# Kernel tuning notes

Measured on AMD Instinct MI355X. Metric: run time of the kernel, lower is better.

Reference implementation:

```python
import math
import jax, jax.numpy as jnp
import numpy as np

N, CH3, T = 64, 192, 2048

def setup_inputs() -> dict:
    key = jax.random.key(0)
    qkv = jax.random.normal(key, (N, CH3, T), dtype=jnp.float32)
    return {"qkv": qkv}

def reference(qkv):
    ch = qkv.shape[1] // 3
    q, k, v = jnp.split(qkv, 3, axis=1)  # each [b, c, t]
    scale = 1.0 / math.sqrt(math.sqrt(ch))
    # [b, t, s] score matrix (faithful to the naive implementation)
    weight = jnp.einsum('bct,bcs->bts', q * scale, k * scale)
    weight = jax.nn.softmax(weight.astype(jnp.float32), axis=-1).astype(weight.dtype)
    return jnp.einsum('bts,bcs->bct', weight, v)
```

## Files before the change

### kernel.cpp

```cpp
#include <hip/hip_runtime.h>
#include <math.h>


#define B_     64
#define CH_    64
#define T_     2048
#define TQ     128
#define SB     64
#define NIT    (T_ / SB)
#define TILE_E 4096

typedef __attribute__((ext_vector_type(8))) short short8;
typedef __attribute__((ext_vector_type(4))) float f32x4;
typedef __attribute__((ext_vector_type(16))) float f32x16;
typedef __attribute__((ext_vector_type(4))) unsigned short us4;
typedef __attribute__((ext_vector_type(8))) unsigned short us8;

static __device__ __forceinline__ unsigned short f2bf(float f) {
    union { float f; unsigned u; } v; v.f = f;
    unsigned r = v.u + 0x7FFFu + ((v.u >> 16) & 1u);
    return (unsigned short)(r >> 16);
}

static __device__ __forceinline__ short8 ld_contig(const unsigned short* p) {
    return *(const short8*)p;
}

static __device__ __forceinline__ short8 ld_strided(const unsigned short* p, int stride) {
    short8 r;
#pragma unroll
    for (int j = 0; j < 8; ++j) r[j] = (short)p[j * stride];
    return r;
}

static __device__ __forceinline__ void gl_lds16(const unsigned short* g, unsigned short* l) {
    __builtin_amdgcn_global_load_lds(
        (const __attribute__((address_space(1))) unsigned int*)g,
        (__attribute__((address_space(3))) unsigned int*)l, 16, 0, 0);
}

static __device__ __forceinline__ float vexp2(float x) {
#if __has_builtin(__builtin_amdgcn_exp2f)
    return __builtin_amdgcn_exp2f(x);
#else
    float r;
    asm("v_exp_f32 %0, %1\n\ts_nop 1" : "=v"(r) : "v"(x));
    return r;
#endif
}

static __device__ __forceinline__ unsigned cvtpk(float lo, float hi) {
    unsigned r;
    asm("v_cvt_pk_bf16_f32 %0, %1, %2" : "=v"(r) : "v"(lo), "v"(hi));
    return r;
}

static __device__ __forceinline__ void pl32(unsigned& a, unsigned& b) {
    asm("v_permlane32_swap_b32 %0, %1" : "+v"(a), "+v"(b));
}

static __device__ __forceinline__ void pl_swap(unsigned& a, unsigned& b) {
    asm("v_permlane32_swap_b32 %0, %1" : "+v"(a), "+v"(b));
    asm("v_permlane16_swap_b32 %0, %1" : "+v"(a), "+v"(b));
}

__global__ __launch_bounds__(256) void qkv_prep(const float* __restrict__ qkv,
                                                unsigned short* __restrict__ Ktg,
                                                unsigned short* __restrict__ Vbg)
{
    __shared__ float Tl[64][65];
    const int tid = threadIdx.x;
    const int b   = blockIdx.x >> 5;
    const int st  = blockIdx.x & 31;
    const int s0  = st * 64;
    const float* Kp = qkv + (size_t)b * (3 * CH_ * T_) + (size_t)CH_ * T_;
    const float* Vp = Kp + (size_t)CH_ * T_;
    const size_t tbase = (size_t)(b * 32 + st) * TILE_E;

    {
        const int c = tid & 63, fq = tid >> 6;
#pragma unroll
        for (int k = 0; k < 4; ++k) {
            const int tl = 16 * fq + 4 * k;
            const float4 v = *(const float4*)(Kp + (size_t)c * T_ + s0 + tl);
            Tl[c][tl] = v.x; Tl[c][tl + 1] = v.y; Tl[c][tl + 2] = v.z; Tl[c][tl + 3] = v.w;
        }
    }

    {
        const int c = tid >> 2, tq = (tid & 3) * 16;
        unsigned short* vout = Vbg + (size_t)b * CH_ * T_ + (size_t)c * T_ + s0 + tq;
        const float* vin = Vp + (size_t)c * T_ + s0 + tq;
#pragma unroll
        for (int k = 0; k < 2; ++k) {
            const float4 a  = *(const float4*)(vin + 8 * k);
            const float4 bq = *(const float4*)(vin + 8 * k + 4);
            us8 w8;
            w8[0]=f2bf(a.x);  w8[1]=f2bf(a.y);  w8[2]=f2bf(a.z);  w8[3]=f2bf(a.w);
            w8[4]=f2bf(bq.x); w8[5]=f2bf(bq.y); w8[6]=f2bf(bq.z); w8[7]=f2bf(bq.w);
            *(us8*)(vout + 8 * k) = w8;
        }
    }
    __syncthreads();

    {
#pragma unroll
        for (int j2 = 0; j2 < 2; ++j2) {
            const int o = j2 * 256 + tid;
            const int R = j2 * 32 + (tid & 31);
            const int g = 2 * (tid >> 6) + ((tid >> 5) & 1);
            us8 w8;
#pragma unroll
            for (int j = 0; j < 8; ++j) w8[j] = f2bf(Tl[8 * g + j][R]);
            *(us8*)(Ktg + tbase + (size_t)o * 8) = w8;
        }
    }
}

__global__ __launch_bounds__(256, 4) void qkv_attn12(const float* __restrict__ qkv,
                                                     const unsigned short* __restrict__ Ktg,
                                                     const unsigned short* __restrict__ Vbg,
                                                     float* __restrict__ out)
{
    __shared__ unsigned short Ks[2][TILE_E];
    __shared__ unsigned short Vs[2][TILE_E];

    const int tid  = threadIdx.x;
    const int lane = tid & 63;
    const int wid  = tid >> 6;
    const int l31  = lane & 31;
    const int hi   = lane >> 5;

    int bid = blockIdx.x;
    bid = (bid & 7) * 128 + (bid >> 3);
    const int b  = bid >> 4;
    const int t0 = (bid & 15) * TQ;
    const int tb = t0 + wid * 32;

    const float* Qp = qkv + (size_t)b * (3 * CH_ * T_);
    const unsigned short* Ktb = Ktg + (size_t)b * 32 * TILE_E;
    const unsigned short* Vbb = Vbg + (size_t)b * (CH_ * T_);

    const int sw7 = l31 & 7;
    int kofs[4];
#pragma unroll
    for (int k = 0; k < 4; ++k) kofs[k] = 8 * ((2 * k + hi) ^ sw7);
    const int rbase = l31 * 64;

    const unsigned short* ksrc = Ktb + (size_t)tid * 8;
    const int lrd = lane * 8;

    const int r0 = tid >> 3;
    const int kx = (tid & 7) ^ (r0 & 7);
    const unsigned short* vsrc0 = Vbb + (size_t)r0 * T_ + 8 * kx;

    short8 aq[4];
#pragma unroll
    for (int ks = 0; ks < 4; ++ks) {
        short8 q;
#pragma unroll
        for (int j = 0; j < 8; ++j)
            q[j] = (short)f2bf(0.180336880f *
                    Qp[(size_t)(16 * ks + 8 * hi + j) * T_ + tb + l31]);
        aq[ks] = q;
    }

    f32x16 zero16;
#pragma unroll
    for (int r = 0; r < 16; ++r) zero16[r] = 0.0f;
    f32x16 o0 = zero16, o1 = zero16;
    float dsum = 0.0f;

    gl_lds16(ksrc,                    &Ks[0][wid * 512]);
    gl_lds16(ksrc + 2048,             &Ks[0][2048 + wid * 512]);
    gl_lds16(vsrc0,                   &Vs[0][wid * 512]);
    gl_lds16(vsrc0 + (size_t)32 * T_, &Vs[0][2048 + wid * 512]);

    for (int it = 0; it < NIT; ++it) {
        __syncthreads();
        const int buf = it & 1;
        if (it + 1 < NIT) {
            const int s1 = (it + 1) * SB;
            const int bo = (buf ^ 1) * TILE_E;
            const unsigned short* kn = ksrc + (size_t)(it + 1) * TILE_E;
            gl_lds16(kn,                           &Ks[0][bo + wid * 512]);
            gl_lds16(kn + 2048,                    &Ks[0][bo + 2048 + wid * 512]);
            gl_lds16(vsrc0 + s1,                   &Vs[0][bo + wid * 512]);
            gl_lds16(vsrc0 + (size_t)32 * T_ + s1, &Vs[0][bo + 2048 + wid * 512]);
        }
        const unsigned short* kb = &Ks[buf][0];
        const unsigned short* vb = &Vs[buf][0];

        __builtin_amdgcn_s_setprio(1);

        f32x16 w0 = zero16, w1 = zero16;
#pragma unroll
        for (int ks = 0; ks < 4; ++ks) {
            const short8 k0 = ld_contig(kb + ks * 512 + lrd);
            const short8 k1 = ld_contig(kb + 2048 + ks * 512 + lrd);
            w0 = __builtin_amdgcn_mfma_f32_32x32x16_bf16(k0, aq[ks], w0, 0, 0, 0);
            w1 = __builtin_amdgcn_mfma_f32_32x32x16_bf16(k1, aq[ks], w1, 0, 0, 0);
        }

#pragma unroll
        for (int st = 0; st < 2; ++st) {
            float e[16];
#pragma unroll
            for (int r = 0; r < 16; ++r) e[r] = vexp2(st ? w1[r] : w0[r]);
            dsum += (((e[0] + e[1]) + (e[2] + e[3])) + ((e[4] + e[5]) + (e[6] + e[7])))
                  + (((e[8] + e[9]) + (e[10] + e[11])) + ((e[12] + e[13]) + (e[14] + e[15])));
            unsigned P0 = cvtpk(e[0], e[1]);
            unsigned P1 = cvtpk(e[2], e[3]);
            unsigned P2 = cvtpk(e[4], e[5]);
            unsigned P3 = cvtpk(e[6], e[7]);
            unsigned P4 = cvtpk(e[8], e[9]);
            unsigned P5 = cvtpk(e[10], e[11]);
            unsigned P6 = cvtpk(e[12], e[13]);
            unsigned P7 = cvtpk(e[14], e[15]);
            pl32(P0, P2);
            pl32(P1, P3);
            pl32(P4, P6);
            pl32(P5, P7);
            union { short8 s8; unsigned u[4]; } pba, pbb;
            pba.u[0] = P0; pba.u[1] = P1; pba.u[2] = P2; pba.u[3] = P3;
            pbb.u[0] = P4; pbb.u[1] = P5; pbb.u[2] = P6; pbb.u[3] = P7;
            const short8 va0 = ld_contig(vb + rbase + kofs[2 * st]);
            const short8 va1 = ld_contig(vb + rbase + kofs[2 * st + 1]);
            const short8 vb0 = ld_contig(vb + 2048 + rbase + kofs[2 * st]);
            const short8 vb1 = ld_contig(vb + 2048 + rbase + kofs[2 * st + 1]);
            o0 = __builtin_amdgcn_mfma_f32_32x32x16_bf16(va0, pba.s8, o0, 0, 0, 0);
            o0 = __builtin_amdgcn_mfma_f32_32x32x16_bf16(va1, pbb.s8, o0, 0, 0, 0);
            o1 = __builtin_amdgcn_mfma_f32_32x32x16_bf16(vb0, pba.s8, o1, 0, 0, 0);
            o1 = __builtin_amdgcn_mfma_f32_32x32x16_bf16(vb1, pbb.s8, o1, 0, 0, 0);
        }
        __builtin_amdgcn_s_setprio(0);
    }

    float d = dsum + __shfl_xor(dsum, 32, 64);
    const float inv = 1.0f / d;

    float* outp = out + (size_t)b * CH_ * T_;
#pragma unroll
    for (int r = 0; r < 16; ++r) {
        const int crow = (r & 3) + 8 * (r >> 2) + 4 * hi;
        outp[(size_t)crow * T_ + tb + l31]        = o0[r] * inv;
        outp[(size_t)(32 + crow) * T_ + tb + l31] = o1[r] * inv;
    }
}

__global__ __launch_bounds__(256) void qkv_attn_fb(const float* __restrict__ qkv,
                                                   float* __restrict__ out)
{
    __shared__ unsigned short Qs[CH_][68];
    __shared__ unsigned short Ksf[CH_][68];
    __shared__ unsigned short Vsf[CH_][72];
    __shared__ unsigned short Psf[4][64][18];

    const int tid  = threadIdx.x;
    const int lane = tid & 63;
    const int wid  = tid >> 6;
    const int l15  = lane & 15;
    const int h    = lane >> 4;
    const int bidx = blockIdx.x;
    const int b    = bidx >> 5;
    const int t0   = (bidx & 31) * 64;
    const int tw   = wid * 16;

    const float* Qp = qkv + (size_t)b * (3 * CH_ * T_);
    const float* Kp = Qp + CH_ * T_;
    const float* Vp = Kp + CH_ * T_;

    const int srow = tid >> 4;
    const int scol = (tid & 15) << 2;

#pragma unroll
    for (int i = 0; i < 4; ++i) {
        const int c = srow + 16 * i;
        const float4 q = *(const float4*)(Qp + (size_t)c * T_ + t0 + scol);
        us4 w; w[0] = f2bf(q.x); w[1] = f2bf(q.y); w[2] = f2bf(q.z); w[3] = f2bf(q.w);
        *(us4*)(&Qs[c][scol]) = w;
    }
    __syncthreads();

    const short8 aq0 = ld_strided(&Qs[0 + 8 * h][tw + l15], 68);
    const short8 aq1 = ld_strided(&Qs[32 + 8 * h][tw + l15], 68);

    short8 aones;
#pragma unroll
    for (int j = 0; j < 8; ++j) aones[j] = (short)0x3F80;

    f32x4 o[4];
#pragma unroll
    for (int cs = 0; cs < 4; ++cs) o[cs] = (f32x4){0.f, 0.f, 0.f, 0.f};
    float l_run = 0.0f;
    const f32x4 zero4 = {0.f, 0.f, 0.f, 0.f};

    for (int it = 0; it < 32; ++it) {
        const int s0 = it * 64;
        __syncthreads();
#pragma unroll
        for (int i = 0; i < 4; ++i) {
            const int c = srow + 16 * i;
            const float4 kv = *(const float4*)(Kp + (size_t)c * T_ + s0 + scol);
            us4 wk; wk[0] = f2bf(kv.x); wk[1] = f2bf(kv.y); wk[2] = f2bf(kv.z); wk[3] = f2bf(kv.w);
            *(us4*)(&Ksf[c][scol]) = wk;
            const float4 vv = *(const float4*)(Vp + (size_t)c * T_ + s0 + scol);
            us4 wv; wv[0] = f2bf(vv.x); wv[1] = f2bf(vv.y); wv[2] = f2bf(vv.z); wv[3] = f2bf(vv.w);
            *(us4*)(&Vsf[c][scol]) = wv;
        }
        __syncthreads();

        f32x4 w[4];
#pragma unroll
        for (int ss = 0; ss < 4; ++ss) {
            const short8 bkl = ld_strided(&Ksf[0 + 8 * h][ss * 16 + l15], 68);
            const short8 bkh = ld_strided(&Ksf[32 + 8 * h][ss * 16 + l15], 68);
            f32x4 acc = zero4;
            acc = __builtin_amdgcn_mfma_f32_16x16x32_bf16(aq0, bkl, acc, 0, 0, 0);
            acc = __builtin_amdgcn_mfma_f32_16x16x32_bf16(aq1, bkh, acc, 0, 0, 0);
            w[ss] = acc;
        }

#pragma unroll
        for (int ss = 0; ss < 4; ++ss) {
            const float e0 = __expf(0.125f * w[ss][0]);
            const float e1 = __expf(0.125f * w[ss][1]);
            const float e2 = __expf(0.125f * w[ss][2]);
            const float e3 = __expf(0.125f * w[ss][3]);
            const unsigned p01 = (unsigned)f2bf(e0) | ((unsigned)f2bf(e1) << 16);
            const unsigned p23 = (unsigned)f2bf(e2) | ((unsigned)f2bf(e3) << 16);
            const int s = ss * 16 + l15;
            *(unsigned*)(&Psf[wid][s][4 * h]) = p01;
            *(unsigned*)(&Psf[wid][s][4 * h + 2]) = p23;
        }

        const short8 pb0 = ld_strided(&Psf[wid][0 + 8 * h][l15], 18);
        const short8 pb1 = ld_strided(&Psf[wid][32 + 8 * h][l15], 18);

        f32x4 lacc = zero4;
        lacc = __builtin_amdgcn_mfma_f32_16x16x32_bf16(aones, pb0, lacc, 0, 0, 0);
        lacc = __builtin_amdgcn_mfma_f32_16x16x32_bf16(aones, pb1, lacc, 0, 0, 0);
        l_run += lacc[0];

#pragma unroll
        for (int cs = 0; cs < 4; ++cs) {
            us4 lo0 = *(const us4*)(&Vsf[cs * 16 + l15][0 + 8 * h]);
            us4 hi0 = *(const us4*)(&Vsf[cs * 16 + l15][4 + 8 * h]);
            us4 lo1 = *(const us4*)(&Vsf[cs * 16 + l15][32 + 8 * h]);
            us4 hi1 = *(const us4*)(&Vsf[cs * 16 + l15][36 + 8 * h]);
            short8 av0, av1;
            av0[0]=(short)lo0[0]; av0[1]=(short)lo0[1]; av0[2]=(short)lo0[2]; av0[3]=(short)lo0[3];
            av0[4]=(short)hi0[0]; av0[5]=(short)hi0[1]; av0[6]=(short)hi0[2]; av0[7]=(short)hi0[3];
            av1[0]=(short)lo1[0]; av1[1]=(short)lo1[1]; av1[2]=(short)lo1[2]; av1[3]=(short)lo1[3];
            av1[4]=(short)hi1[0]; av1[5]=(short)hi1[1]; av1[6]=(short)hi1[2]; av1[7]=(short)hi1[3];
            o[cs] = __builtin_amdgcn_mfma_f32_16x16x32_bf16(av0, pb0, o[cs], 0, 0, 0);
            o[cs] = __builtin_amdgcn_mfma_f32_16x16x32_bf16(av1, pb1, o[cs], 0, 0, 0);
        }
    }

    const float invd = 1.0f / l_run;
    float* outp = out + (size_t)b * CH_ * T_;
#pragma unroll
    for (int cs = 0; cs < 4; ++cs)
#pragma unroll
        for (int r = 0; r < 4; ++r)
            outp[(size_t)(cs * 16 + 4 * h + r) * T_ + t0 + tw + l15] = o[cs][r] * invd;
}

extern "C" void kernel_launch(void* const* d_in, const int* in_sizes, int n_in,
                              void* d_out, int out_size, void* d_ws, size_t ws_size,
                              hipStream_t stream) {
    const float* qkv = (const float*)d_in[0];
    float* outp = (float*)d_out;
    const size_t need = (size_t)2 * B_ * CH_ * T_ * sizeof(unsigned short);
    if (ws_size >= need) {
        unsigned short* Ktg = (unsigned short*)d_ws;
        unsigned short* Vbg = Ktg + (size_t)B_ * T_ * CH_;
        qkv_prep<<<dim3(B_ * 32), dim3(256), 0, stream>>>(qkv, Ktg, Vbg);
        qkv_attn12<<<dim3(B_ * (T_ / TQ)), dim3(256), 0, stream>>>(qkv, Ktg, Vbg, outp);
    } else {
        qkv_attn_fb<<<dim3(B_ * 32), dim3(256), 0, stream>>>(qkv, outp);
    }
}
```

Before: 95.44 us.

## Pre-tile V in MFMA fragment layout and load it directly from global

The prep kernel now writes V in a per-tile layout that matches the MFMA operand fragments, the same way K is already stored. The attention kernel drops the V shared-memory double buffer and loads V fragments straight from global (L2/cache) into registers, issued early in each iteration. This removes LDS traffic and LDS footprint for V, which could allow higher occupancy. In exchange, global-load latency now sits on the critical path with no explicit prefetch into LDS.

```diff
diff --git a/kernel.cpp b/kernel.cpp
--- a/kernel.cpp
+++ b/kernel.cpp
@@ -23,6 +23,10 @@
 }
 
 static __device__ __forceinline__ short8 ld_contig(const unsigned short* p) {
+    return *(const short8*)p;
+}
+
+static __device__ __forceinline__ short8 ld_g16(const unsigned short* p) {
     return *(const short8*)p;
 }
 
@@ -88,18 +92,21 @@
     }
 
     {
-        const int c = tid >> 2, tq = (tid & 3) * 16;
-        unsigned short* vout = Vbg + (size_t)b * CH_ * T_ + (size_t)c * T_ + s0 + tq;
-        const float* vin = Vp + (size_t)c * T_ + s0 + tq;
-#pragma unroll
-        for (int k = 0; k < 2; ++k) {
-            const float4 a  = *(const float4*)(vin + 8 * k);
-            const float4 bq = *(const float4*)(vin + 8 * k + 4);
-            us8 w8;
-            w8[0]=f2bf(a.x);  w8[1]=f2bf(a.y);  w8[2]=f2bf(a.z);  w8[3]=f2bf(a.w);
-            w8[4]=f2bf(bq.x); w8[5]=f2bf(bq.y); w8[6]=f2bf(bq.z); w8[7]=f2bf(bq.w);
-            *(us8*)(vout + 8 * k) = w8;
-        }
+        const int R = tid >> 2;
+        const int m = tid & 3;
+        const float* vin = Vp + (size_t)R * T_ + s0 + 16 * m;
+        const float4 a0 = *(const float4*)(vin);
+        const float4 a1 = *(const float4*)(vin + 4);
+        const float4 a2 = *(const float4*)(vin + 8);
+        const float4 a3 = *(const float4*)(vin + 12);
+        us8 w0, w1;
+        w0[0]=f2bf(a0.x); w0[1]=f2bf(a0.y); w0[2]=f2bf(a0.z); w0[3]=f2bf(a0.w);
+        w0[4]=f2bf(a1.x); w0[5]=f2bf(a1.y); w0[6]=f2bf(a1.z); w0[7]=f2bf(a1.w);
+        w1[0]=f2bf(a2.x); w1[1]=f2bf(a2.y); w1[2]=f2bf(a2.z); w1[3]=f2bf(a2.w);
+        w1[4]=f2bf(a3.x); w1[5]=f2bf(a3.y); w1[6]=f2bf(a3.z); w1[7]=f2bf(a3.w);
+        const int o = ((R >> 5) << 8) + (m << 6) + (R & 31);
+        *(us8*)(Vbg + tbase + (size_t)o * 8)        = w0;
+        *(us8*)(Vbg + tbase + (size_t)(o + 32) * 8) = w1;
     }
     __syncthreads();
 
@@ -117,13 +124,12 @@
     }
 }
 
-__global__ __launch_bounds__(256, 4) void qkv_attn12(const float* __restrict__ qkv,
+__global__ __launch_bounds__(256, 4) void qkv_attn13(const float* __restrict__ qkv,
                                                      const unsigned short* __restrict__ Ktg,
                                                      const unsigned short* __restrict__ Vbg,
                                                      float* __restrict__ out)
 {
     __shared__ unsigned short Ks[2][TILE_E];
-    __shared__ unsigned short Vs[2][TILE_E];
 
     const int tid  = threadIdx.x;
     const int lane = tid & 63;
@@ -139,20 +145,12 @@
 
     const float* Qp = qkv + (size_t)b * (3 * CH_ * T_);
     const unsigned short* Ktb = Ktg + (size_t)b * 32 * TILE_E;
-    const unsigned short* Vbb = Vbg + (size_t)b * (CH_ * T_);
-
-    const int sw7 = l31 & 7;
-    int kofs[4];
-#pragma unroll
-    for (int k = 0; k < 4; ++k) kofs[k] = 8 * ((2 * k + hi) ^ sw7);
-    const int rbase = l31 * 64;
+    const unsigned short* Vtb = Vbg + (size_t)b * 32 * TILE_E;
 
     const unsigned short* ksrc = Ktb + (size_t)tid * 8;
     const int lrd = lane * 8;
 
-    const int r0 = tid >> 3;
-    const int kx = (tid & 7) ^ (r0 & 7);
-    const unsigned short* vsrc0 = Vbb + (size_t)r0 * T_ + 8 * kx;
+    const unsigned short* vit = Vtb + lrd;
 
     short8 aq[4];
 #pragma unroll
@@ -171,27 +169,26 @@
     f32x16 o0 = zero16, o1 = zero16;
     float dsum = 0.0f;
 
-    gl_lds16(ksrc,                    &Ks[0][wid * 512]);
-    gl_lds16(ksrc + 2048,             &Ks[0][2048 + wid * 512]);
-    gl_lds16(vsrc0,                   &Vs[0][wid * 512]);
-    gl_lds16(vsrc0 + (size_t)32 * T_, &Vs[0][2048 + wid * 512]);
+    gl_lds16(ksrc,        &Ks[0][wid * 512]);
+    gl_lds16(ksrc + 2048, &Ks[0][2048 + wid * 512]);
 
     for (int it = 0; it < NIT; ++it) {
         __syncthreads();
         const int buf = it & 1;
         if (it + 1 < NIT) {
-            const int s1 = (it + 1) * SB;
+            const unsigned short* kn = ksrc + (size_t)(it + 1) * TILE_E;
             const int bo = (buf ^ 1) * TILE_E;
-            const unsigned short* kn = ksrc + (size_t)(it + 1) * TILE_E;
-            gl_lds16(kn,                           &Ks[0][bo + wid * 512]);
-            gl_lds16(kn + 2048,                    &Ks[0][bo + 2048 + wid * 512]);
-            gl_lds16(vsrc0 + s1,                   &Vs[0][bo + wid * 512]);
-            gl_lds16(vsrc0 + (size_t)32 * T_ + s1, &Vs[0][bo + 2048 + wid * 512]);
+            gl_lds16(kn,        &Ks[0][bo + wid * 512]);
+            gl_lds16(kn + 2048, &Ks[0][bo + 2048 + wid * 512]);
         }
         const unsigned short* kb = &Ks[buf][0];
-        const unsigned short* vb = &Vs[buf][0];
 
         __builtin_amdgcn_s_setprio(1);
+
+        const short8 vA0 = ld_g16(vit);
+        const short8 vA1 = ld_g16(vit + 512);
+        const short8 vB0 = ld_g16(vit + 2048);
+        const short8 vB1 = ld_g16(vit + 2048 + 512);
 
         f32x16 w0 = zero16, w1 = zero16;
 #pragma unroll
@@ -202,11 +199,10 @@
             w1 = __builtin_amdgcn_mfma_f32_32x32x16_bf16(k1, aq[ks], w1, 0, 0, 0);
         }
 
-#pragma unroll
-        for (int st = 0; st < 2; ++st) {
+        {
             float e[16];
 #pragma unroll
-            for (int r = 0; r < 16; ++r) e[r] = vexp2(st ? w1[r] : w0[r]);
+            for (int r = 0; r < 16; ++r) e[r] = vexp2(w0[r]);
             dsum += (((e[0] + e[1]) + (e[2] + e[3])) + ((e[4] + e[5]) + (e[6] + e[7])))
                   + (((e[8] + e[9]) + (e[10] + e[11])) + ((e[12] + e[13]) + (e[14] + e[15])));
             unsigned P0 = cvtpk(e[0], e[1]);
@@ -224,16 +220,45 @@
             union { short8 s8; unsigned u[4]; } pba, pbb;
             pba.u[0] = P0; pba.u[1] = P1; pba.u[2] = P2; pba.u[3] = P3;
             pbb.u[0] = P4; pbb.u[1] = P5; pbb.u[2] = P6; pbb.u[3] = P7;
-            const short8 va0 = ld_contig(vb + rbase + kofs[2 * st]);
-            const short8 va1 = ld_contig(vb + rbase + kofs[2 * st + 1]);
-            const short8 vb0 = ld_contig(vb + 2048 + rbase + kofs[2 * st]);
-            const short8 vb1 = ld_contig(vb + 2048 + rbase + kofs[2 * st + 1]);
-            o0 = __builtin_amdgcn_mfma_f32_32x32x16_bf16(va0, pba.s8, o0, 0, 0, 0);
-            o0 = __builtin_amdgcn_mfma_f32_32x32x16_bf16(va1, pbb.s8, o0, 0, 0, 0);
-            o1 = __builtin_amdgcn_mfma_f32_32x32x16_bf16(vb0, pba.s8, o1, 0, 0, 0);
-            o1 = __builtin_amdgcn_mfma_f32_32x32x16_bf16(vb1, pbb.s8, o1, 0, 0, 0);
+            o0 = __builtin_amdgcn_mfma_f32_32x32x16_bf16(vA0, pba.s8, o0, 0, 0, 0);
+            o0 = __builtin_amdgcn_mfma_f32_32x32x16_bf16(vA1, pbb.s8, o0, 0, 0, 0);
+            o1 = __builtin_amdgcn_mfma_f32_32x32x16_bf16(vB0, pba.s8, o1, 0, 0, 0);
+            o1 = __builtin_amdgcn_mfma_f32_32x32x16_bf16(vB1, pbb.s8, o1, 0, 0, 0);
+        }
+
+        {
+            const short8 vC0 = ld_g16(vit + 1024);
+            const short8 vC1 = ld_g16(vit + 1536);
+            const short8 vD0 = ld_g16(vit + 2048 + 1024);
+            const short8 vD1 = ld_g16(vit + 2048 + 1536);
+            float e[16];
+#pragma unroll
+            for (int r = 0; r < 16; ++r) e[r] = vexp2(w1[r]);
+            dsum += (((e[0] + e[1]) + (e[2] + e[3])) + ((e[4] + e[5]) + (e[6] + e[7])))
+                  + (((e[8] + e[9]) + (e[10] + e[11])) + ((e[12] + e[13]) + (e[14] + e[15])));
+            unsigned P0 = cvtpk(e[0], e[1]);
+            unsigned P1 = cvtpk(e[2], e[3]);
+            unsigned P2 = cvtpk(e[4], e[5]);
+            unsigned P3 = cvtpk(e[6], e[7]);
+            unsigned P4 = cvtpk(e[8], e[9]);
+            unsigned P5 = cvtpk(e[10], e[11]);
+            unsigned P6 = cvtpk(e[12], e[13]);
+            unsigned P7 = cvtpk(e[14], e[15]);
+            pl32(P0, P2);
+            pl32(P1, P3);
+            pl32(P4, P6);
+            pl32(P5, P7);
+            union { short8 s8; unsigned u[4]; } pba, pbb;
+            pba.u[0] = P0; pba.u[1] = P1; pba.u[2] = P2; pba.u[3] = P3;
+            pbb.u[0] = P4; pbb.u[1] = P5; pbb.u[2] = P6; pbb.u[3] = P7;
+            o0 = __builtin_amdgcn_mfma_f32_32x32x16_bf16(vC0, pba.s8, o0, 0, 0, 0);
+            o0 = __builtin_amdgcn_mfma_f32_32x32x16_bf16(vC1, pbb.s8, o0, 0, 0, 0);
+            o1 = __builtin_amdgcn_mfma_f32_32x32x16_bf16(vD0, pba.s8, o1, 0, 0, 0);
+            o1 = __builtin_amdgcn_mfma_f32_32x32x16_bf16(vD1, pbb.s8, o1, 0, 0, 0);
         }
         __builtin_amdgcn_s_setprio(0);
+
+        vit += TILE_E;
     }
 
     float d = dsum + __shfl_xor(dsum, 32, 64);
@@ -377,7 +402,7 @@
         unsigned short* Ktg = (unsigned short*)d_ws;
         unsigned short* Vbg = Ktg + (size_t)B_ * T_ * CH_;
         qkv_prep<<<dim3(B_ * 32), dim3(256), 0, stream>>>(qkv, Ktg, Vbg);
-        qkv_attn12<<<dim3(B_ * (T_ / TQ)), dim3(256), 0, stream>>>(qkv, Ktg, Vbg, outp);
+        qkv_attn13<<<dim3(B_ * (T_ / TQ)), dim3(256), 0, stream>>>(qkv, Ktg, Vbg, outp);
     } else {
         qkv_attn_fb<<<dim3(B_ * 32), dim3(256), 0, stream>>>(qkv, outp);
     }
```

Result: slower. 98.60 us (+3.3%).
